# Kernel optimization log

Measured on AMD Instinct MI355X. Metric: run time of the kernel, lower is better.

Reference implementation:

```python
import jax, jax.numpy as jnp
import numpy as np

D_MODEL = 2048
D_STATE = 128
D_CONV = 4
EXPAND = 2
HEADDIM = 64
CHUNK = 64
D_INNER = EXPAND * D_MODEL            # 4096
NHEADS = D_INNER // HEADDIM           # 64
CONV_DIM = D_INNER + 2 * D_STATE      # 4352
D_IN_PROJ = 2 * D_INNER + 2 * D_STATE + NHEADS  # 8512
BATCH, SEQLEN = 2, 2048


def segsum(x):
    """Stable segment sum. x: (..., T) -> (..., T, T)."""
    T = x.shape[-1]
    xx = jnp.broadcast_to(x[..., :, None], x.shape + (T,))  # [.., d, e] = x[.., d]
    mask_lower = jnp.tril(jnp.ones((T, T), dtype=bool), -1)
    s = jnp.cumsum(jnp.where(mask_lower, xx, 0.0), axis=-2)
    mask_diag = jnp.tril(jnp.ones((T, T), dtype=bool), 0)
    return jnp.where(mask_diag, s, -jnp.inf)


def ssd(x, A, Bm, Cm, chunk):
    """x: [b,L,h,p], A: [b,L,h], Bm/Cm: [b,L,n]."""
    b, L, h, p = x.shape
    c = L // chunk
    x = x.reshape(b, c, chunk, h, p)
    A = A.reshape(b, c, chunk, h).transpose(0, 3, 1, 2)     # b h c l
    Bm = Bm.reshape(b, c, chunk, -1)                         # b c l n
    Cm = Cm.reshape(b, c, chunk, -1)
    A_cum = jnp.cumsum(A, axis=-1)                           # b h c l
    Lmat = jnp.exp(segsum(A))                                # b h c l s
    # intra-chunk (diagonal) output
    Y_diag = jnp.einsum('bcln,bcsn,bhcls,bcshp->bclhp', Cm, Bm, Lmat, x)
    # per-chunk states
    decay_states = jnp.exp(A_cum[..., -1:] - A_cum)          # b h c l
    states = jnp.einsum('bcln,bhcl,bclhp->bchpn', Bm, decay_states, x)
    init = jnp.zeros_like(states[:, :1])
    states = jnp.concatenate([init, states], axis=1)         # b (c+1) h p n
    # inter-chunk recurrence via segsum over chunk-level decays
    A_last = jnp.pad(A_cum[..., -1], ((0, 0), (0, 0), (1, 0)))  # b h (c+1)
    decay_chunk = jnp.exp(segsum(A_last))                    # b h (c+1) (c+1)
    new_states = jnp.einsum('bhzc,bchpn->bzhpn', decay_chunk, states)
    states, final_state = new_states[:, :-1], new_states[:, -1]
    # state -> output
    out_decay = jnp.exp(A_cum)                               # b h c l
    Y_off = jnp.einsum('bcln,bchpn,bhcl->bclhp', Cm, states, out_decay)
    return (Y_diag + Y_off).reshape(b, L, h, p), final_state


def setup_inputs() -> dict:
    key = jax.random.key(0)
    ks = jax.random.split(key, 8)
    u = jax.random.normal(ks[0], (BATCH, SEQLEN, D_MODEL), jnp.float32)
    W_in = jax.random.normal(ks[1], (D_MODEL, D_IN_PROJ), jnp.float32) / np.sqrt(D_MODEL).astype(np.float32)
    conv_w = jax.random.normal(ks[2], (CONV_DIM, D_CONV), jnp.float32) * np.sqrt(2.0 / D_CONV).astype(np.float32)
    conv_b = jnp.zeros((CONV_DIM,), jnp.float32)
    dt_bias = jax.random.uniform(ks[3], (NHEADS,), jnp.float32, minval=-2.0, maxval=2.0)
    A_log = jax.random.normal(ks[4], (NHEADS,), jnp.float32) * 0.1
    D_param = jnp.ones((NHEADS,), jnp.float32)
    norm_w = jnp.ones((D_INNER,), jnp.float32)
    W_out = jax.random.normal(ks[5], (D_INNER, D_MODEL), jnp.float32) / np.sqrt(D_INNER).astype(np.float32)
    return {'u': u, 'W_in': W_in, 'conv_w': conv_w, 'conv_b': conv_b,
            'dt_bias': dt_bias, 'A_log': A_log, 'D_param': D_param,
            'norm_w': norm_w, 'W_out': W_out}


def reference(u, W_in, conv_w, conv_b, dt_bias, A_log, D_param, norm_w, W_out):
    b, L, _ = u.shape
    zxbcdt = u @ W_in                                        # [b, L, 2*din + 2*n + h]
    z = zxbcdt[..., :D_INNER]
    xBC = zxbcdt[..., D_INNER:D_INNER + CONV_DIM]
    dt = zxbcdt[..., D_INNER + CONV_DIM:]
    dt = jax.nn.softplus(dt + dt_bias)                       # [b, L, h]
    # causal depthwise conv1d (kernel D_CONV, groups=channels)
    xp = jnp.pad(xBC, ((0, 0), (D_CONV - 1, 0), (0, 0)))
    xBC = sum(xp[:, w:w + L, :] * conv_w[:, w] for w in range(D_CONV)) + conv_b
    xBC = jax.nn.silu(xBC)
    x = xBC[..., :D_INNER]
    Bm = xBC[..., D_INNER:D_INNER + D_STATE]                 # [b, L, n]
    Cm = xBC[..., D_INNER + D_STATE:]                        # [b, L, n]
    x = x.reshape(b, L, NHEADS, HEADDIM)
    A = -jnp.exp(A_log)                                      # [h]
    y, final_state = ssd(x * dt[..., None], A * dt, Bm, Cm, CHUNK)
    y = y + x * D_param[:, None]                             # skip term
    y = y.reshape(b, L, D_INNER)
    # gated RMSNorm (fp32)
    yf = y * jax.nn.silu(z)
    rrms = jax.lax.rsqrt(jnp.mean(yf * yf, axis=-1, keepdims=True) + 1e-5)
    y = yf * rrms * norm_w
    return y @ W_out
```

## Files before the change

kernel.cpp:

```cpp
#include <hip/hip_runtime.h>

typedef unsigned short u16;
typedef __attribute__((ext_vector_type(8))) short bhalf8;
typedef __attribute__((ext_vector_type(4))) float floatx4;

__device__ __forceinline__ u16 f2bf(float f) {
    union { float f; unsigned u; } v; v.f = f;
    unsigned u = v.u;
    unsigned r = u + 0x7fffu + ((u >> 16) & 1u);
    return (u16)(r >> 16);
}
__device__ __forceinline__ float b2f(u16 h) {
    union { unsigned u; float f; } v; v.u = ((unsigned)h) << 16; return v.f;
}
__device__ __forceinline__ void unpack2(unsigned u, float& lo, float& hi) {
    union { unsigned u; float f; } a, b;
    a.u = u << 16; b.u = u & 0xffff0000u;
    lo = a.f; hi = b.f;
}
__device__ __forceinline__ void load_lds16(const void* g, void* l) {
    __builtin_amdgcn_global_load_lds(
        (const __attribute__((address_space(1))) unsigned int*)g,
        (__attribute__((address_space(3))) unsigned int*)l, 16, 0, 0);
}

__global__ void k_f2b4(const float* __restrict__ in, u16* __restrict__ out, int n4) {
    int i = blockIdx.x * 256 + threadIdx.x;
    if (i < n4) {
        float4 v = ((const float4*)in)[i];
        unsigned lo = (unsigned)f2bf(v.x) | ((unsigned)f2bf(v.y) << 16);
        unsigned hi = (unsigned)f2bf(v.z) | ((unsigned)f2bf(v.w) << 16);
        ((uint2*)out)[i] = make_uint2(lo, hi);
    }
}

__global__ void k_transpose_f2b(const float* __restrict__ W, u16* __restrict__ Wt,
                                int K, int N) {
    __shared__ float tile[32][33];
    int nt = blockIdx.x * 32, kt = blockIdx.y * 32;
    int tx = threadIdx.x, ty = threadIdx.y;
    #pragma unroll
    for (int r = 0; r < 32; r += 8) {
        int k = kt + ty + r, n = nt + tx;
        tile[ty + r][tx] = (n < N && k < K) ? W[(size_t)k * N + n] : 0.f;
    }
    __syncthreads();
    #pragma unroll
    for (int r = 0; r < 32; r += 8) {
        int n = nt + ty + r, k = kt + tx;
        Wt[(size_t)n * K + k] = f2bf(tile[tx][ty + r]);
    }
}

template <int EPI>
__global__ __launch_bounds__(256) void gemm_bt(
    const u16* __restrict__ A, const u16* __restrict__ Bt, int M, int N, int K,
    int NT, int GM, int NBW,
    float* __restrict__ outF,
    u16* __restrict__ zb, u16* __restrict__ xbc, float* __restrict__ dtq,
    const float* __restrict__ dt_bias) {
    __shared__ u16 As[128 * 64];
    __shared__ u16 Bs[128 * 64];
    int t = threadIdx.x;
    int w = t >> 6, lane = t & 63;
    int nwg = gridDim.x, bid = blockIdx.x;
    int swz = (bid & 7) * (nwg >> 3) + (bid >> 3);
    int sup = GM * NT;
    int g = swz / sup, r0 = swz % sup;
    int nb = r0 / (GM * NBW);
    int rem = r0 - nb * (GM * NBW);
    int gw = NT - nb * NBW; if (gw > NBW) gw = NBW;
    int nf = rem % gw, mi = rem / gw;
    int n_t = nb * NBW + nf, m_t = g * GM + mi;
    int m0 = m_t * 128, n0 = n_t * 128;
    int wm = (w >> 1) * 64, wn = (w & 1) * 64;
    floatx4 acc[4][4];
    #pragma unroll
    for (int i = 0; i < 4; i++)
        #pragma unroll
        for (int j = 0; j < 4; j++) acc[i][j] = (floatx4){0.f, 0.f, 0.f, 0.f};

    for (int k0 = 0; k0 < K; k0 += 64) {
        #pragma unroll
        for (int i = 0; i < 4; i++) {
            int c = w * 4 + i;
            int byte = c * 1024 + lane * 16;
            int row = byte >> 7;
            int colb = (byte & 127) ^ ((row & 7) << 4);
            load_lds16(A + (size_t)(m0 + row) * K + k0 + (colb >> 1), (char*)As + byte);
            load_lds16(Bt + (size_t)(n0 + row) * K + k0 + (colb >> 1), (char*)Bs + byte);
        }
        __syncthreads();
        #pragma unroll
        for (int ks = 0; ks < 2; ks++) {
            int kk = ks * 32 + ((lane >> 4) << 3);
            bhalf8 af[4], bf[4];
            #pragma unroll
            for (int mi2 = 0; mi2 < 4; mi2++) {
                int row = wm + mi2 * 16 + (lane & 15);
                int idx = (row * 64 + kk) ^ ((row & 7) << 3);
                af[mi2] = *(const bhalf8*)(As + idx);
            }
            #pragma unroll
            for (int ni = 0; ni < 4; ni++) {
                int col = wn + ni * 16 + (lane & 15);
                int idx = (col * 64 + kk) ^ ((col & 7) << 3);
                bf[ni] = *(const bhalf8*)(Bs + idx);
            }
            #pragma unroll
            for (int mi2 = 0; mi2 < 4; mi2++)
                #pragma unroll
                for (int ni = 0; ni < 4; ni++)
                    acc[mi2][ni] = __builtin_amdgcn_mfma_f32_16x16x32_bf16(
                        af[mi2], bf[ni], acc[mi2][ni], 0, 0, 0);
        }
        __syncthreads();
    }
    #pragma unroll
    for (int mi2 = 0; mi2 < 4; mi2++) {
        #pragma unroll
        for (int ni = 0; ni < 4; ni++) {
            floatx4 v = acc[mi2][ni];
            int col = n0 + wn + ni * 16 + (lane & 15);
            #pragma unroll
            for (int r = 0; r < 4; r++) {
                int row = m0 + wm + mi2 * 16 + ((lane >> 4) << 2) + r;
                float val = v[r];
                if (EPI == 0) {
                    outF[(size_t)row * N + col] = val;
                } else {
                    if (col < 4096) {
                        zb[(size_t)row * 4096 + col] = f2bf(val);
                    } else if (col < 8448) {
                        xbc[(size_t)row * 4352 + (col - 4096)] = f2bf(val);
                    } else if (col < 8512) {
                        int h = col - 8448;
                        float xv = val + dt_bias[h];
                        float sp = (xv > 20.f) ? xv : log1pf(__expf(xv));
                        dtq[(size_t)row * 64 + h] = sp;
                    }
                }
            }
        }
    }
}

__global__ __launch_bounds__(256) void k_conv(
    const u16* __restrict__ xbc, const float* __restrict__ conv_w,
    const float* __restrict__ conv_b,
    u16* __restrict__ x, u16* __restrict__ Bo, u16* __restrict__ Co) {
    int bid = blockIdx.x;
    int b = bid >> 8, lt = bid & 255;
    int l0 = lt * 8;
    size_t rb = (size_t)(b * 2048) * 4352;
    for (int ch = threadIdx.x; ch < 4352; ch += 256) {
        float w0 = conv_w[ch * 4 + 0], w1 = conv_w[ch * 4 + 1];
        float w2 = conv_w[ch * 4 + 2], w3 = conv_w[ch * 4 + 3];
        float bc = conv_b[ch];
        float h0 = (l0 >= 3) ? b2f(xbc[rb + (size_t)(l0 - 3) * 4352 + ch]) : 0.f;
        float h1 = (l0 >= 2) ? b2f(xbc[rb + (size_t)(l0 - 2) * 4352 + ch]) : 0.f;
        float h2 = (l0 >= 1) ? b2f(xbc[rb + (size_t)(l0 - 1) * 4352 + ch]) : 0.f;
        #pragma unroll
        for (int i = 0; i < 8; i++) {
            int l = l0 + i;
            float xc = b2f(xbc[rb + (size_t)l * 4352 + ch]);
            float acc = bc + w0 * h0 + w1 * h1 + w2 * h2 + w3 * xc;
            float v = acc / (1.f + __expf(-acc));
            int row = b * 2048 + l;
            if (ch < 4096) {
                x[(size_t)row * 4096 + ch] = f2bf(v);
            } else if (ch < 4224) {
                Bo[(size_t)row * 128 + (ch - 4096)] = f2bf(v);
            } else {
                Co[(size_t)row * 128 + (ch - 4224)] = f2bf(v);
            }
            h0 = h1; h1 = h2; h2 = xc;
        }
    }
}

__global__ void k_dtprep(const float* __restrict__ dtq, const float* __restrict__ A_log,
                         float* __restrict__ acum, float* __restrict__ Tc) {
    int bc = blockIdx.x;
    int h = threadIdx.x;
    float A = -__expf(A_log[h]);
    float s = 0.f;
    #pragma unroll
    for (int l = 0; l < 64; l++) {
        int row = bc * 64 + l;
        s += A * dtq[row * 64 + h];
        acum[(size_t)row * 64 + h] = s;
    }
    int b = bc >> 5, c = bc & 31;
    Tc[(b * 64 + h) * 32 + c] = s;
}

__global__ __launch_bounds__(256) void k_G(const u16* __restrict__ Bo, const u16* __restrict__ Co,
                                           float* __restrict__ G) {
    int bc = blockIdx.x;
    int lq = blockIdx.y;
    __shared__ float BsT[128][68];
    __shared__ float Cs[16][132];
    int t = threadIdx.x;
    for (int idx = t; idx < 64 * 128; idx += 256) {
        int r = idx >> 7, n = idx & 127;
        BsT[n][r] = b2f(Bo[(size_t)(bc * 64 + r) * 128 + n]);
    }
    for (int idx = t; idx < 16 * 128; idx += 256) {
        int r = idx >> 7, n = idx & 127;
        Cs[r][n] = b2f(Co[(size_t)(bc * 64 + lq * 16 + r) * 128 + n]);
    }
    __syncthreads();
    int lr = t >> 4, sq = t & 15;
    int l = lq * 16 + lr;
    float a[4] = {0.f, 0.f, 0.f, 0.f};
    for (int n = 0; n < 128; n++) {
        float cv = Cs[lr][n];
        const float4* bp = (const float4*)&BsT[n][sq * 4];
        float4 b0 = bp[0];
        a[0] += cv * b0.x; a[1] += cv * b0.y; a[2] += cv * b0.z; a[3] += cv * b0.w;
    }
    size_t gb = ((size_t)bc * 64 + l) * 64 + sq * 4;
    #pragma unroll
    for (int i = 0; i < 4; i++) G[gb + i] = a[i];
}

__global__ __launch_bounds__(256) void k_diag(
    const u16* __restrict__ xb, const u16* __restrict__ Bo,
    const float* __restrict__ G, const float* __restrict__ acum,
    const float* __restrict__ dtq,
    u16* __restrict__ y, u16* __restrict__ cs) {
    int bc = blockIdx.x, h = blockIdx.y;
    __shared__ u16 XT[4096];
    __shared__ u16 Pl[4096];
    __shared__ u16 BTd[8192];
    __shared__ float ac[64], dec[64], dts[64];
    int t = threadIdx.x, w = t >> 6, lane = t & 63;
    if (t < 64) {
        ac[t] = acum[(size_t)(bc * 64 + t) * 64 + h];
        dts[t] = dtq[(size_t)(bc * 64 + t) * 64 + h];
    }
    __syncthreads();
    if (t < 64) dec[t] = __expf(ac[63] - ac[t]);
    for (int idx = t; idx < 4096; idx += 256) {
        int s = idx >> 6, p = idx & 63;
        float v = b2f(xb[(size_t)(bc * 64 + s) * 4096 + h * 64 + p]) * dts[s];
        XT[(p << 6) + (s ^ ((p & 7) << 3))] = f2bf(v);
    }
    for (int idx = t; idx < 4096; idx += 256) {
        int l = idx >> 6, s = idx & 63;
        float v = (s <= l) ? __expf(ac[l] - ac[s]) * G[((size_t)bc * 64 + l) * 64 + s] : 0.f;
        Pl[(l << 6) + (s ^ ((l & 7) << 3))] = f2bf(v);
    }
    __syncthreads();
    for (int idx = t; idx < 8192; idx += 256) {
        int l = idx >> 7, n = idx & 127;
        float v = b2f(Bo[(size_t)(bc * 64 + l) * 128 + n]) * dec[l];
        BTd[(n << 6) + (l ^ ((n & 7) << 3))] = f2bf(v);
    }
    __syncthreads();
    {
        floatx4 accY[4];
        #pragma unroll
        for (int ni = 0; ni < 4; ni++) accY[ni] = (floatx4){0.f, 0.f, 0.f, 0.f};
        int row = (w << 4) + (lane & 15);
        #pragma unroll
        for (int ks = 0; ks < 2; ks++) {
            int k = (ks << 5) + ((lane >> 4) << 3);
            int kx = k ^ ((row & 7) << 3);
            bhalf8 af = *(const bhalf8*)(Pl + (row << 6) + kx);
            #pragma unroll
            for (int ni = 0; ni < 4; ni++) {
                int pr = (ni << 4) + (lane & 15);
                bhalf8 bf = *(const bhalf8*)(XT + (pr << 6) + kx);
                accY[ni] = __builtin_amdgcn_mfma_f32_16x16x32_bf16(af, bf, accY[ni], 0, 0, 0);
            }
        }
        #pragma unroll
        for (int ni = 0; ni < 4; ni++) {
            int col = (ni << 4) + (lane & 15);
            #pragma unroll
            for (int r = 0; r < 4; r++) {
                int l = (w << 4) + ((lane >> 4) << 2) + r;
                y[(size_t)(bc * 64 + l) * 4096 + h * 64 + col] = f2bf(accY[ni][r]);
            }
        }
    }
    {
        floatx4 accS[8];
        #pragma unroll
        for (int ni = 0; ni < 8; ni++) accS[ni] = (floatx4){0.f, 0.f, 0.f, 0.f};
        int prow = (w << 4) + (lane & 15);
        #pragma unroll
        for (int ks = 0; ks < 2; ks++) {
            int k = (ks << 5) + ((lane >> 4) << 3);
            int kx = k ^ ((prow & 7) << 3);
            bhalf8 af = *(const bhalf8*)(XT + (prow << 6) + kx);
            #pragma unroll
            for (int ni = 0; ni < 8; ni++) {
                int nr = (ni << 4) + (lane & 15);
                bhalf8 bf = *(const bhalf8*)(BTd + (nr << 6) + kx);
                accS[ni] = __builtin_amdgcn_mfma_f32_16x16x32_bf16(af, bf, accS[ni], 0, 0, 0);
            }
        }
        #pragma unroll
        for (int ni = 0; ni < 8; ni++) {
            int n = (ni << 4) + (lane & 15);
            #pragma unroll
            for (int r = 0; r < 4; r++) {
                int p = (w << 4) + ((lane >> 4) << 2) + r;
                cs[((size_t)(bc * 64 + h) * 64 + p) * 128 + n] = f2bf(accS[ni][r]);
            }
        }
    }
}

__global__ __launch_bounds__(256) void k_scan(u16* __restrict__ cs, const float* __restrict__ Tc) {
    int bid = blockIdx.x;
    int bh = bid >> 5, pb = bid & 31;
    int b = bh >> 6, h = bh & 63;
    int pn = pb * 256 + threadIdx.x;
    const float* Tp = Tc + bh * 32;
    size_t stride = (size_t)64 * 8192;
    size_t base = (((size_t)(b * 32) * 64) + h) * 8192 + pn;
    float v[32];
    #pragma unroll
    for (int c = 0; c < 32; c++) v[c] = b2f(cs[base + (size_t)c * stride]);
    float P = 0.f;
    #pragma unroll
    for (int c = 0; c < 32; c++) {
        float tmp = v[c];
        cs[base + (size_t)c * stride] = f2bf(P);
        P = __expf(Tp[c]) * P + tmp;
    }
}

__global__ __launch_bounds__(256) void k_yoff(
    const u16* __restrict__ Co, const u16* __restrict__ cs,
    const float* __restrict__ acum, u16* __restrict__ y) {
    int bc = blockIdx.x, h = blockIdx.y;
    __shared__ u16 Cl[8192];
    __shared__ u16 Sl[8192];
    __shared__ float od[64];
    int t = threadIdx.x, w = t >> 6, lane = t & 63;
    for (int idx = t; idx < 8192; idx += 256) {
        int l = idx >> 7, n = idx & 127;
        Cl[(l << 7) + (n ^ ((l & 15) << 3))] = Co[(size_t)(bc * 64 + l) * 128 + n];
    }
    size_t pbase = ((size_t)bc * 64 + h) * 8192;
    for (int idx = t; idx < 8192; idx += 256) {
        int p = idx >> 7, n = idx & 127;
        Sl[(p << 7) + (n ^ ((p & 15) << 3))] = cs[pbase + idx];
    }
    if (t < 64) od[t] = __expf(acum[(size_t)(bc * 64 + t) * 64 + h]);
    __syncthreads();
    floatx4 acc[4];
    #pragma unroll
    for (int ni = 0; ni < 4; ni++) acc[ni] = (floatx4){0.f, 0.f, 0.f, 0.f};
    int lrow = (w << 4) + (lane & 15);
    #pragma unroll
    for (int ks = 0; ks < 4; ks++) {
        int k = (ks << 5) + ((lane >> 4) << 3);
        int kx = k ^ ((lrow & 15) << 3);
        bhalf8 af = *(const bhalf8*)(Cl + (lrow << 7) + kx);
        #pragma unroll
        for (int ni = 0; ni < 4; ni++) {
            int pr = (ni << 4) + (lane & 15);
            bhalf8 bf = *(const bhalf8*)(Sl + (pr << 7) + kx);
            acc[ni] = __builtin_amdgcn_mfma_f32_16x16x32_bf16(af, bf, acc[ni], 0, 0, 0);
        }
    }
    #pragma unroll
    for (int ni = 0; ni < 4; ni++) {
        int col = (ni << 4) + (lane & 15);
        #pragma unroll
        for (int r = 0; r < 4; r++) {
            int l = (w << 4) + ((lane >> 4) << 2) + r;
            size_t yi = (size_t)(bc * 64 + l) * 4096 + h * 64 + col;
            y[yi] = f2bf(b2f(y[yi]) + od[l] * acc[ni][r]);
        }
    }
}

__global__ __launch_bounds__(256) void k_norm(
    const u16* __restrict__ y, const u16* __restrict__ x, const u16* __restrict__ z,
    const float* __restrict__ D_param, const float* __restrict__ norm_w,
    u16* __restrict__ ynorm) {
    int row = blockIdx.x;
    int t = threadIdx.x;
    size_t base = (size_t)row * 4096 + (size_t)t * 16;
    float yv[16], xf[16], zf[16];
    {
        uint4 a = ((const uint4*)(y + base))[0];
        uint4 b = ((const uint4*)(y + base))[1];
        unpack2(a.x, yv[0], yv[1]); unpack2(a.y, yv[2], yv[3]);
        unpack2(a.z, yv[4], yv[5]); unpack2(a.w, yv[6], yv[7]);
        unpack2(b.x, yv[8], yv[9]); unpack2(b.y, yv[10], yv[11]);
        unpack2(b.z, yv[12], yv[13]); unpack2(b.w, yv[14], yv[15]);
    }
    {
        uint4 a = ((const uint4*)(x + base))[0];
        uint4 b = ((const uint4*)(x + base))[1];
        unpack2(a.x, xf[0], xf[1]); unpack2(a.y, xf[2], xf[3]);
        unpack2(a.z, xf[4], xf[5]); unpack2(a.w, xf[6], xf[7]);
        unpack2(b.x, xf[8], xf[9]); unpack2(b.y, xf[10], xf[11]);
        unpack2(b.z, xf[12], xf[13]); unpack2(b.w, xf[14], xf[15]);
    }
    {
        uint4 a = ((const uint4*)(z + base))[0];
        uint4 b = ((const uint4*)(z + base))[1];
        unpack2(a.x, zf[0], zf[1]); unpack2(a.y, zf[2], zf[3]);
        unpack2(a.z, zf[4], zf[5]); unpack2(a.w, zf[6], zf[7]);
        unpack2(b.x, zf[8], zf[9]); unpack2(b.y, zf[10], zf[11]);
        unpack2(b.z, zf[12], zf[13]); unpack2(b.w, zf[14], zf[15]);
    }
    float D = D_param[t >> 2];
    float vals[16], ss = 0.f;
    #pragma unroll
    for (int j = 0; j < 16; j++) {
        float v = yv[j] + xf[j] * D;
        float zz = zf[j];
        float yf = v * (zz / (1.f + __expf(-zz)));
        vals[j] = yf;
        ss += yf * yf;
    }
    #pragma unroll
    for (int o = 32; o > 0; o >>= 1) ss += __shfl_down(ss, o, 64);
    __shared__ float red[4];
    if ((t & 63) == 0) red[t >> 6] = ss;
    __syncthreads();
    float tot = red[0] + red[1] + red[2] + red[3];
    float rr = rsqrtf(tot * (1.f / 4096.f) + 1e-5f);
    unsigned o32[8];
    #pragma unroll
    for (int j = 0; j < 8; j++) {
        float lo = vals[2 * j] * rr * norm_w[t * 16 + 2 * j];
        float hi = vals[2 * j + 1] * rr * norm_w[t * 16 + 2 * j + 1];
        o32[j] = (unsigned)f2bf(lo) | ((unsigned)f2bf(hi) << 16);
    }
    uint4 w0, w1;
    w0.x = o32[0]; w0.y = o32[1]; w0.z = o32[2]; w0.w = o32[3];
    w1.x = o32[4]; w1.y = o32[5]; w1.z = o32[6]; w1.w = o32[7];
    ((uint4*)(ynorm + base))[0] = w0;
    ((uint4*)(ynorm + base))[1] = w1;
}

extern "C" void kernel_launch(void* const* d_in, const int* in_sizes, int n_in,
                              void* d_out, int out_size, void* d_ws, size_t ws_size,
                              hipStream_t stream) {
    const float* u       = (const float*)d_in[0];
    const float* W_in    = (const float*)d_in[1];
    const float* conv_w  = (const float*)d_in[2];
    const float* conv_b  = (const float*)d_in[3];
    const float* dt_bias = (const float*)d_in[4];
    const float* A_log   = (const float*)d_in[5];
    const float* D_param = (const float*)d_in[6];
    const float* norm_w  = (const float*)d_in[7];
    const float* W_out   = (const float*)d_in[8];
    float* out = (float*)d_out;

    const size_t REGION = (size_t)134217728;
    size_t need = REGION
                + (size_t)33554432
                + (size_t)33554432
                + (size_t)1048576
                + (size_t)1048576
                + (size_t)1048576
                + (size_t)16384
                + (size_t)1048576
                + (size_t)1048576
                + (size_t)33554432;
    if (ws_size < need) return;

    char* ws = (char*)d_ws;
    u16*   ubf   = (u16*)(ws);
    u16*   WinT  = (u16*)(ws + 16777216);
    u16*   xbc   = (u16*)(ws + 16777216 + 35651584);
    u16*   cs    = (u16*)(ws);
    u16*   WoutT = (u16*)(ws);
    u16*   ynorm = (u16*)(ws + 16777216);
    char* p = ws + REGION;
    u16*   zb    = (u16*)p;            p += 33554432;
    u16*   xb    = (u16*)p;            p += 33554432;
    u16*   Bo    = (u16*)p;            p += 1048576;
    u16*   Co    = (u16*)p;            p += 1048576;
    float* acum  = (float*)p;          p += 1048576;
    float* Tc    = (float*)p;          p += 16384;
    float* G     = (float*)p;          p += 1048576;
    float* dtq   = (float*)p;          p += 1048576;
    u16*   yb    = (u16*)p;            p += 33554432;

    k_f2b4<<<8192, 256, 0, stream>>>(u, ubf, 4096 * 2048 / 4);
    k_transpose_f2b<<<dim3(268, 64), dim3(32, 8), 0, stream>>>(W_in, WinT, 2048, 8512);
    gemm_bt<1><<<2144, 256, 0, stream>>>(ubf, WinT, 4096, 8576, 2048, 67, 4, 8,
                                         nullptr, zb, xbc, dtq, dt_bias);
    k_conv<<<512, 256, 0, stream>>>(xbc, conv_w, conv_b, xb, Bo, Co);
    k_dtprep<<<64, 64, 0, stream>>>(dtq, A_log, acum, Tc);
    k_G<<<dim3(64, 4), 256, 0, stream>>>(Bo, Co, G);
    k_diag<<<dim3(64, 64), 256, 0, stream>>>(xb, Bo, G, acum, dtq, yb, cs);
    k_scan<<<4096, 256, 0, stream>>>(cs, Tc);
    k_yoff<<<dim3(64, 64), 256, 0, stream>>>(Co, cs, acum, yb);
    k_transpose_f2b<<<dim3(64, 128), dim3(32, 8), 0, stream>>>(W_out, WoutT, 4096, 2048);
    k_norm<<<4096, 256, 0, stream>>>(yb, xb, zb, D_param, norm_w, ynorm);
    gemm_bt<0><<<512, 256, 0, stream>>>(ynorm, WoutT, 4096, 2048, 4096, 16, 4, 4,
                                        out, nullptr, nullptr, nullptr, nullptr);
    (void)in_sizes; (void)n_in; (void)out_size;
}
```

Baseline: 663.4 us.

## Double-buffer GEMM LDS tiles and drop XCD/grouped block swizzle

The bf16 GEMM now uses two LDS buffers and issues the next K-tile's global-to-LDS loads before computing on the current one, which removes one barrier per iteration and overlaps memory with MFMA work. It also replaces the XCD-aware grouped tile swizzle with a plain 2D grid mapping. LDS use doubles to 64KB per block, which may lower occupancy. Losing the swizzle may also hurt L2 reuse across the chiplets.

```diff
diff --git a/kernel.cpp b/kernel.cpp
--- a/kernel.cpp
+++ b/kernel.cpp
@@ -55,24 +55,14 @@
 template <int EPI>
 __global__ __launch_bounds__(256) void gemm_bt(
     const u16* __restrict__ A, const u16* __restrict__ Bt, int M, int N, int K,
-    int NT, int GM, int NBW,
     float* __restrict__ outF,
     u16* __restrict__ zb, u16* __restrict__ xbc, float* __restrict__ dtq,
     const float* __restrict__ dt_bias) {
-    __shared__ u16 As[128 * 64];
-    __shared__ u16 Bs[128 * 64];
+    __shared__ u16 As[2 * 8192];
+    __shared__ u16 Bs[2 * 8192];
     int t = threadIdx.x;
     int w = t >> 6, lane = t & 63;
-    int nwg = gridDim.x, bid = blockIdx.x;
-    int swz = (bid & 7) * (nwg >> 3) + (bid >> 3);
-    int sup = GM * NT;
-    int g = swz / sup, r0 = swz % sup;
-    int nb = r0 / (GM * NBW);
-    int rem = r0 - nb * (GM * NBW);
-    int gw = NT - nb * NBW; if (gw > NBW) gw = NBW;
-    int nf = rem % gw, mi = rem / gw;
-    int n_t = nb * NBW + nf, m_t = g * GM + mi;
-    int m0 = m_t * 128, n0 = n_t * 128;
+    int m0 = blockIdx.y * 128, n0 = blockIdx.x * 128;
     int wm = (w >> 1) * 64, wn = (w & 1) * 64;
     floatx4 acc[4][4];
     #pragma unroll
@@ -80,51 +70,64 @@
         #pragma unroll
         for (int j = 0; j < 4; j++) acc[i][j] = (floatx4){0.f, 0.f, 0.f, 0.f};
 
-    for (int k0 = 0; k0 < K; k0 += 64) {
+    const int nt = K >> 6;
+    const int byte0 = (w * 4) * 1024 + lane * 16;
+
+    auto stage = [&](int sel, int k0) {
         #pragma unroll
         for (int i = 0; i < 4; i++) {
-            int c = w * 4 + i;
-            int byte = c * 1024 + lane * 16;
+            int byte = byte0 + i * 1024;
             int row = byte >> 7;
             int colb = (byte & 127) ^ ((row & 7) << 4);
-            load_lds16(A + (size_t)(m0 + row) * K + k0 + (colb >> 1), (char*)As + byte);
-            load_lds16(Bt + (size_t)(n0 + row) * K + k0 + (colb >> 1), (char*)Bs + byte);
-        }
-        __syncthreads();
+            load_lds16(A + (size_t)(m0 + row) * K + k0 + (colb >> 1),
+                       (char*)As + sel * 16384 + byte);
+            load_lds16(Bt + (size_t)(n0 + row) * K + k0 + (colb >> 1),
+                       (char*)Bs + sel * 16384 + byte);
+        }
+    };
+
+    stage(0, 0);
+    __syncthreads();
+    int cur = 0;
+    for (int kt = 0; kt < nt; ++kt) {
+        if (kt + 1 < nt) stage(cur ^ 1, (kt + 1) << 6);
+        const u16* Ab = As + cur * 8192;
+        const u16* Bb = Bs + cur * 8192;
         #pragma unroll
         for (int ks = 0; ks < 2; ks++) {
             int kk = ks * 32 + ((lane >> 4) << 3);
             bhalf8 af[4], bf[4];
             #pragma unroll
-            for (int mi2 = 0; mi2 < 4; mi2++) {
-                int row = wm + mi2 * 16 + (lane & 15);
+            for (int mi = 0; mi < 4; mi++) {
+                int row = wm + mi * 16 + (lane & 15);
                 int idx = (row * 64 + kk) ^ ((row & 7) << 3);
-                af[mi2] = *(const bhalf8*)(As + idx);
+                af[mi] = *(const bhalf8*)(Ab + idx);
             }
             #pragma unroll
             for (int ni = 0; ni < 4; ni++) {
                 int col = wn + ni * 16 + (lane & 15);
                 int idx = (col * 64 + kk) ^ ((col & 7) << 3);
-                bf[ni] = *(const bhalf8*)(Bs + idx);
-            }
-            #pragma unroll
-            for (int mi2 = 0; mi2 < 4; mi2++)
+                bf[ni] = *(const bhalf8*)(Bb + idx);
+            }
+            #pragma unroll
+            for (int mi = 0; mi < 4; mi++)
                 #pragma unroll
                 for (int ni = 0; ni < 4; ni++)
-                    acc[mi2][ni] = __builtin_amdgcn_mfma_f32_16x16x32_bf16(
-                        af[mi2], bf[ni], acc[mi2][ni], 0, 0, 0);
+                    acc[mi][ni] = __builtin_amdgcn_mfma_f32_16x16x32_bf16(
+                        af[mi], bf[ni], acc[mi][ni], 0, 0, 0);
         }
         __syncthreads();
-    }
-    #pragma unroll
-    for (int mi2 = 0; mi2 < 4; mi2++) {
+        cur ^= 1;
+    }
+    #pragma unroll
+    for (int mi = 0; mi < 4; mi++) {
         #pragma unroll
         for (int ni = 0; ni < 4; ni++) {
-            floatx4 v = acc[mi2][ni];
+            floatx4 v = acc[mi][ni];
             int col = n0 + wn + ni * 16 + (lane & 15);
             #pragma unroll
             for (int r = 0; r < 4; r++) {
-                int row = m0 + wm + mi2 * 16 + ((lane >> 4) << 2) + r;
+                int row = m0 + wm + mi * 16 + ((lane >> 4) << 2) + r;
                 float val = v[r];
                 if (EPI == 0) {
                     outF[(size_t)row * N + col] = val;
@@ -492,8 +495,8 @@
 
     k_f2b4<<<8192, 256, 0, stream>>>(u, ubf, 4096 * 2048 / 4);
     k_transpose_f2b<<<dim3(268, 64), dim3(32, 8), 0, stream>>>(W_in, WinT, 2048, 8512);
-    gemm_bt<1><<<2144, 256, 0, stream>>>(ubf, WinT, 4096, 8576, 2048, 67, 4, 8,
-                                         nullptr, zb, xbc, dtq, dt_bias);
+    gemm_bt<1><<<dim3(67, 32), 256, 0, stream>>>(ubf, WinT, 4096, 8576, 2048,
+                                                 nullptr, zb, xbc, dtq, dt_bias);
     k_conv<<<512, 256, 0, stream>>>(xbc, conv_w, conv_b, xb, Bo, Co);
     k_dtprep<<<64, 64, 0, stream>>>(dtq, A_log, acum, Tc);
     k_G<<<dim3(64, 4), 256, 0, stream>>>(Bo, Co, G);
@@ -502,7 +505,7 @@
     k_yoff<<<dim3(64, 64), 256, 0, stream>>>(Co, cs, acum, yb);
     k_transpose_f2b<<<dim3(64, 128), dim3(32, 8), 0, stream>>>(W_out, WoutT, 4096, 2048);
     k_norm<<<4096, 256, 0, stream>>>(yb, xb, zb, D_param, norm_w, ynorm);
-    gemm_bt<0><<<512, 256, 0, stream>>>(ynorm, WoutT, 4096, 2048, 4096, 16, 4, 4,
-                                        out, nullptr, nullptr, nullptr, nullptr);
+    gemm_bt<0><<<dim3(16, 32), 256, 0, stream>>>(ynorm, WoutT, 4096, 2048, 4096,
+                                                 out, nullptr, nullptr, nullptr, nullptr);
     (void)in_sizes; (void)n_in; (void)out_size;
 }
```

Result: faster. 607.0 us, median of 2 (-8.5%).
